# Kernel tuning notes

Measured on AMD Instinct MI355X. Metric: run time of the kernel, lower is better.

Reference implementation:

```python
import jax, jax.numpy as jnp
import numpy as np

TEMPERATURE = 0.5  # init temperature; attn_drop=0.0 so dropout is identity


def setup_inputs() -> dict:
    key = jax.random.key(0)
    k1, k2, k3 = jax.random.split(key, 3)
    B, H, N, D = 4, 8, 2048, 64
    q = jax.random.normal(k1, (B, H, N, D), dtype=jnp.float32)
    k = jax.random.normal(k2, (B, H, N, D), dtype=jnp.float32)
    v = jax.random.normal(k3, (B, H, N, D), dtype=jnp.float32)
    scale = jnp.asarray(D ** -0.5, dtype=jnp.float32)
    return {"q": q, "k": k, "v": v, "scale": scale}


def reference(q, k, v, scale):
    # logits: [B,H,N,N]
    logits = jnp.einsum("bhqd,bhkd->bhqk", q, k) * scale
    # first softmax acts as a soft mask over keys
    soft_mask = jax.nn.softmax(logits / TEMPERATURE, axis=-1)
    # second softmax over masked logits (elementwise product, NOT matmul)
    attn = jax.nn.softmax(logits * soft_mask, axis=-1)
    # dropout with p=0.0 is identity
    out = jnp.einsum("bhqk,bhkd->bhqd", attn, v)
    return out
```

## Files before the change

### kernel.cpp

```cpp
#include <hip/hip_runtime.h>


typedef _Float16 f16;
typedef f16 f16x8 __attribute__((ext_vector_type(8)));
typedef float f32x16 __attribute__((ext_vector_type(16)));

#define MFMA32(a, b, c) __builtin_amdgcn_mfma_f32_32x32x16_f16((a), (b), (c), 0, 0, 0)
#define EXP2(x) __builtin_amdgcn_exp2f(x)

#define N_CTX 2048
#define DH 64
#define KT 64
#define NKT (N_CTX / KT)
#define ROWS 128
#define QS 72
#define HEAD_ELEMS (N_CTX * DH)
#define C2 2.885390081777927f

__device__ inline unsigned pk(float a, float b) {
    typedef __fp16 fp16x2_t __attribute__((ext_vector_type(2)));
    union { fp16x2_t v; unsigned u; } x;
    x.v = __builtin_amdgcn_cvt_pkrtz(a, b);
    return x.u;
}

__device__ inline void load16_lds(const f16* g, f16* l) {
    __builtin_amdgcn_global_load_lds(
        (const __attribute__((address_space(1))) void*)g,
        (__attribute__((address_space(3))) void*)l, 16, 0, 0);
}

__global__ __launch_bounds__(256)
void cvt_kv(const float* __restrict__ k, const float* __restrict__ v,
            f16* __restrict__ ko, f16* __restrict__ vto) {
    __shared__ float Vs[64][65];
    const int bh = blockIdx.x & 31;
    const int kt = blockIdx.x >> 5;
    const int t  = threadIdx.x;
    const float* kb = k + (size_t)bh * HEAD_ELEMS + (size_t)kt * KT * DH;
    f16* kob = ko + (size_t)bh * HEAD_ELEMS + (size_t)kt * KT * DH;
    #pragma unroll
    for (int it = 0; it < 2; ++it) {
        int i = (it * 256 + t) * 8;
        float4 a = *(const float4*)&kb[i];
        float4 b = *(const float4*)&kb[i + 4];
        *(uint4*)&kob[i] = make_uint4(pk(a.x, a.y), pk(a.z, a.w), pk(b.x, b.y), pk(b.z, b.w));
    }
    const float* vb = v + (size_t)bh * HEAD_ELEMS + (size_t)kt * KT * DH;
    #pragma unroll
    for (int it = 0; it < 4; ++it) {
        int idx = it * 256 + t;
        int row = idx >> 4, c4 = idx & 15;
        *(float4*)&Vs[row][c4 * 4] = *(const float4*)&vb[row * DH + c4 * 4];
    }
    __syncthreads();
    int d = t >> 2, sub = t & 3;
    unsigned w[8];
    #pragma unroll
    for (int j = 0; j < 8; ++j) {
        int c = sub * 8 + j;
        w[j] = pk(Vs[c][d], Vs[c + 32][d]);
    }
    f16* ob = vto + (size_t)bh * HEAD_ELEMS + (size_t)d * N_CTX + kt * KT + sub * 16;
    *(uint4*)(ob)     = make_uint4(w[0], w[1], w[2], w[3]);
    *(uint4*)(ob + 8) = make_uint4(w[4], w[5], w[6], w[7]);
}

__global__ __launch_bounds__(256, 2)
void stk_attn_mfma(const float* __restrict__ qg, const f16* __restrict__ kh,
                   const f16* __restrict__ vth, const float* __restrict__ sg,
                   float* __restrict__ og) {
    __shared__ f16 Qs[ROWS * QS];
    __shared__ f16 Ks[2][KT * DH];
    __shared__ f16 Vt[2][DH * KT];
    __shared__ f16 Ps[4][32 * QS];

    const int tid  = threadIdx.x;
    const int wv   = tid >> 6;
    const int lane = tid & 63;
    const int l31  = lane & 31;
    const int lh   = lane >> 5;
    const int bh   = blockIdx.x & 31;
    const int q0   = (blockIdx.x >> 5) * ROWS;
    const float scale2 = sg[0] * C2;

    const float* qb = qg + (size_t)bh * HEAD_ELEMS;
    const f16*   kb = kh + (size_t)bh * HEAD_ELEMS;
    const f16*   vtb = vth + (size_t)bh * HEAD_ELEMS;
    float*       ob = og + (size_t)bh * HEAD_ELEMS;

    #pragma unroll
    for (int it = 0; it < 8; ++it) {
        int idx = it * 256 + tid;
        int row = idx >> 4, c4 = idx & 15;
        float4 v = *(const float4*)&qb[((size_t)(q0 + row)) * DH + c4 * 4];
        *(uint2*)&Qs[row * QS + c4 * 4] =
            make_uint2(pk(v.x * scale2, v.y * scale2), pk(v.z * scale2, v.w * scale2));
    }
    __syncthreads();

    f16x8 aq[4];
    #pragma unroll
    for (int km = 0; km < 4; ++km)
        aq[km] = *(const f16x8*)&Qs[(wv * 32 + l31) * QS + km * 16 + lh * 8];

    const int c0   = (wv * 2) * 64 + lane;
    const int c1   = c0 + 64;
    const int key0 = c0 >> 3, key1 = c1 >> 3;
    const int ks_src0 = key0 * DH + (((c0 & 7) ^ (key0 & 7)) * 8);
    const int ks_src1 = key1 * DH + (((c1 & 7) ^ (key1 & 7)) * 8);
    const long vt_src0 = (long)key0 * N_CTX + (((c0 & 7) ^ (key0 & 7)) * 8);
    const long vt_src1 = (long)key1 * N_CTX + (((c1 & 7) ^ (key1 & 7)) * 8);
    const int dst0 = (wv * 2) * 512, dst1 = dst0 + 512;
    const int x8 = l31 & 7;
    int xo[4];
    #pragma unroll
    for (int km = 0; km < 4; ++km) xo[km] = ((2 * km + lh) ^ x8) * 8;
    const int gb0 = l31 * 64, gb1 = (32 + l31) * 64;
    f16* const ps_wv = &Ps[wv][0];

    float s1[16] = {0};
    load16_lds(kb + ks_src0, &Ks[0][dst0]);
    load16_lds(kb + ks_src1, &Ks[0][dst1]);
    __syncthreads();
    for (int kt = 0; kt < NKT; ++kt) {
        const int cur = kt & 1;
        if (kt + 1 < NKT) {
            const f16* src = kb + (kt + 1) * (KT * DH);
            load16_lds(src + ks_src0, &Ks[cur ^ 1][dst0]);
            load16_lds(src + ks_src1, &Ks[cur ^ 1][dst1]);
        }
        #pragma unroll
        for (int kg = 0; kg < 2; ++kg) {
            const int gb = kg ? gb1 : gb0;
            f32x16 acc;
            #pragma unroll
            for (int i = 0; i < 16; ++i) acc[i] = 0.f;
            #pragma unroll
            for (int km = 0; km < 4; ++km) {
                f16x8 b = *(const f16x8*)&Ks[cur][gb + xo[km]];
                acc = MFMA32(aq[km], b, acc);
            }
            #pragma unroll
            for (int r = 0; r < 16; ++r)
                s1[r] += EXP2(acc[r]);
        }
        __syncthreads();
    }
    float inv1[16];
    #pragma unroll
    for (int r = 0; r < 16; ++r) {
        float v = s1[r];
        v += __shfl_xor(v, 1, 64);
        v += __shfl_xor(v, 2, 64);
        v += __shfl_xor(v, 4, 64);
        v += __shfl_xor(v, 8, 64);
        v += __shfl_xor(v, 16, 64);
        inv1[r] = 0.5f / v;
    }

    float l2[16] = {0};
    f32x16 O0, O1;
    #pragma unroll
    for (int i = 0; i < 16; ++i) { O0[i] = 0.f; O1[i] = 0.f; }

    load16_lds(kb + ks_src0, &Ks[0][dst0]);
    load16_lds(kb + ks_src1, &Ks[0][dst1]);
    load16_lds(vtb + vt_src0, &Vt[0][dst0]);
    load16_lds(vtb + vt_src1, &Vt[0][dst1]);
    __syncthreads();
    for (int kt = 0; kt < NKT; ++kt) {
        const int cur = kt & 1;
        if (kt + 1 < NKT) {
            const f16* src = kb + (kt + 1) * (KT * DH);
            load16_lds(src + ks_src0, &Ks[cur ^ 1][dst0]);
            load16_lds(src + ks_src1, &Ks[cur ^ 1][dst1]);
            load16_lds(vtb + vt_src0 + (kt + 1) * KT, &Vt[cur ^ 1][dst0]);
            load16_lds(vtb + vt_src1 + (kt + 1) * KT, &Vt[cur ^ 1][dst1]);
        }
        f32x16 a0, a1;
        #pragma unroll
        for (int i = 0; i < 16; ++i) { a0[i] = 0.f; a1[i] = 0.f; }
        #pragma unroll
        for (int km = 0; km < 4; ++km) {
            f16x8 b0 = *(const f16x8*)&Ks[cur][gb0 + xo[km]];
            f16x8 b1 = *(const f16x8*)&Ks[cur][gb1 + xo[km]];
            a0 = MFMA32(aq[km], b0, a0);
            a1 = MFMA32(aq[km], b1, a1);
        }
        #pragma unroll
        for (int r = 0; r < 16; ++r) {
            int row_r = (r & 3) + 8 * (r >> 2) + 4 * lh;
            float e10 = EXP2(a0[r]);
            float e20 = EXP2((a0[r] * e10) * inv1[r]);
            float e11 = EXP2(a1[r]);
            float e21 = EXP2((a1[r] * e11) * inv1[r]);
            l2[r] += e20 + e21;
            *(unsigned*)&ps_wv[row_r * QS + 2 * l31] = pk(e20, e21);
        }
        #pragma unroll
        for (int km = 0; km < 4; ++km) {
            f16x8 ap = *(const f16x8*)&ps_wv[l31 * QS + km * 16 + lh * 8];
            f16x8 bv0 = *(const f16x8*)&Vt[cur][gb0 + xo[km]];
            f16x8 bv1 = *(const f16x8*)&Vt[cur][gb1 + xo[km]];
            O0 = MFMA32(ap, bv0, O0);
            O1 = MFMA32(ap, bv1, O1);
        }
        __syncthreads();
    }

    float invl2[16];
    #pragma unroll
    for (int r = 0; r < 16; ++r) {
        float v = l2[r];
        v += __shfl_xor(v, 1, 64);
        v += __shfl_xor(v, 2, 64);
        v += __shfl_xor(v, 4, 64);
        v += __shfl_xor(v, 8, 64);
        v += __shfl_xor(v, 16, 64);
        invl2[r] = 1.0f / v;
    }
    #pragma unroll
    for (int r = 0; r < 16; ++r) {
        int row = q0 + wv * 32 + (r & 3) + 8 * (r >> 2) + 4 * lh;
        ob[(size_t)row * DH + l31]      = O0[r] * invl2[r];
        ob[(size_t)row * DH + 32 + l31] = O1[r] * invl2[r];
    }
}

extern "C" void kernel_launch(void* const* d_in, const int* in_sizes, int n_in,
                              void* d_out, int out_size, void* d_ws, size_t ws_size,
                              hipStream_t stream) {
    const float* q = (const float*)d_in[0];
    const float* k = (const float*)d_in[1];
    const float* v = (const float*)d_in[2];
    const float* s = (const float*)d_in[3];
    float* out = (float*)d_out;
    f16* kf  = (f16*)d_ws;
    f16* vtf = (f16*)((char*)d_ws + 8388608);
    cvt_kv<<<1024, 256, 0, stream>>>(k, v, kf, vtf);
    dim3 grid(32 * 16);
    stk_attn_mfma<<<grid, 256, 0, stream>>>(q, kf, vtf, s, out);
}
```

Measured before the change: 177.5 us.

## Double query rows per block to 256 and alias the P buffer onto Q staging

Each block now processes 256 query rows with 8 waves (512 threads) instead of 128 rows with 4 waves. This halves the grid and halves the K/V tile traffic per query row, since each thread now issues one async LDS load per tile instead of two. The per-wave P buffer is aliased onto the Q staging region, which is no longer needed once Q is held in registers, so LDS use stays within budget. The tradeoff is 256 blocks for a 256-CU-class GPU, which gives only about one block per CU, so latency hiding depends on having 8 waves per block.

```diff
diff --git a/kernel.cpp b/kernel.cpp
--- a/kernel.cpp
+++ b/kernel.cpp
@@ -12,7 +12,7 @@
 #define DH 64
 #define KT 64
 #define NKT (N_CTX / KT)
-#define ROWS 128
+#define ROWS 256
 #define QS 72
 #define HEAD_ELEMS (N_CTX * DH)
 #define C2 2.885390081777927f
@@ -66,14 +66,13 @@
     *(uint4*)(ob + 8) = make_uint4(w[4], w[5], w[6], w[7]);
 }
 
-__global__ __launch_bounds__(256, 2)
+__global__ __launch_bounds__(512, 4)
 void stk_attn_mfma(const float* __restrict__ qg, const f16* __restrict__ kh,
                    const f16* __restrict__ vth, const float* __restrict__ sg,
                    float* __restrict__ og) {
-    __shared__ f16 Qs[ROWS * QS];
+    __shared__ f16 QsPs[ROWS * QS];
     __shared__ f16 Ks[2][KT * DH];
     __shared__ f16 Vt[2][DH * KT];
-    __shared__ f16 Ps[4][32 * QS];
 
     const int tid  = threadIdx.x;
     const int wv   = tid >> 6;
@@ -91,10 +90,10 @@
 
     #pragma unroll
     for (int it = 0; it < 8; ++it) {
-        int idx = it * 256 + tid;
+        int idx = it * 512 + tid;
         int row = idx >> 4, c4 = idx & 15;
         float4 v = *(const float4*)&qb[((size_t)(q0 + row)) * DH + c4 * 4];
-        *(uint2*)&Qs[row * QS + c4 * 4] =
+        *(uint2*)&QsPs[row * QS + c4 * 4] =
             make_uint2(pk(v.x * scale2, v.y * scale2), pk(v.z * scale2, v.w * scale2));
     }
     __syncthreads();
@@ -102,34 +101,28 @@
     f16x8 aq[4];
     #pragma unroll
     for (int km = 0; km < 4; ++km)
-        aq[km] = *(const f16x8*)&Qs[(wv * 32 + l31) * QS + km * 16 + lh * 8];
-
-    const int c0   = (wv * 2) * 64 + lane;
-    const int c1   = c0 + 64;
-    const int key0 = c0 >> 3, key1 = c1 >> 3;
-    const int ks_src0 = key0 * DH + (((c0 & 7) ^ (key0 & 7)) * 8);
-    const int ks_src1 = key1 * DH + (((c1 & 7) ^ (key1 & 7)) * 8);
-    const long vt_src0 = (long)key0 * N_CTX + (((c0 & 7) ^ (key0 & 7)) * 8);
-    const long vt_src1 = (long)key1 * N_CTX + (((c1 & 7) ^ (key1 & 7)) * 8);
-    const int dst0 = (wv * 2) * 512, dst1 = dst0 + 512;
+        aq[km] = *(const f16x8*)&QsPs[(wv * 32 + l31) * QS + km * 16 + lh * 8];
+
+    const int c0   = wv * 64 + lane;
+    const int key0 = c0 >> 3;
+    const int swz  = ((c0 & 7) ^ (key0 & 7)) * 8;
+    const int ks_src0 = key0 * DH + swz;
+    const long vt_src0 = (long)key0 * N_CTX + swz;
+    const int dst0 = wv * 512;
     const int x8 = l31 & 7;
     int xo[4];
     #pragma unroll
     for (int km = 0; km < 4; ++km) xo[km] = ((2 * km + lh) ^ x8) * 8;
     const int gb0 = l31 * 64, gb1 = (32 + l31) * 64;
-    f16* const ps_wv = &Ps[wv][0];
+    f16* const ps_wv = &QsPs[wv * 32 * QS];
 
     float s1[16] = {0};
     load16_lds(kb + ks_src0, &Ks[0][dst0]);
-    load16_lds(kb + ks_src1, &Ks[0][dst1]);
     __syncthreads();
     for (int kt = 0; kt < NKT; ++kt) {
         const int cur = kt & 1;
-        if (kt + 1 < NKT) {
-            const f16* src = kb + (kt + 1) * (KT * DH);
-            load16_lds(src + ks_src0, &Ks[cur ^ 1][dst0]);
-            load16_lds(src + ks_src1, &Ks[cur ^ 1][dst1]);
-        }
+        if (kt + 1 < NKT)
+            load16_lds(kb + (kt + 1) * (KT * DH) + ks_src0, &Ks[cur ^ 1][dst0]);
         #pragma unroll
         for (int kg = 0; kg < 2; ++kg) {
             const int gb = kg ? gb1 : gb0;
@@ -165,18 +158,13 @@
     for (int i = 0; i < 16; ++i) { O0[i] = 0.f; O1[i] = 0.f; }
 
     load16_lds(kb + ks_src0, &Ks[0][dst0]);
-    load16_lds(kb + ks_src1, &Ks[0][dst1]);
     load16_lds(vtb + vt_src0, &Vt[0][dst0]);
-    load16_lds(vtb + vt_src1, &Vt[0][dst1]);
     __syncthreads();
     for (int kt = 0; kt < NKT; ++kt) {
         const int cur = kt & 1;
         if (kt + 1 < NKT) {
-            const f16* src = kb + (kt + 1) * (KT * DH);
-            load16_lds(src + ks_src0, &Ks[cur ^ 1][dst0]);
-            load16_lds(src + ks_src1, &Ks[cur ^ 1][dst1]);
+            load16_lds(kb + (kt + 1) * (KT * DH) + ks_src0, &Ks[cur ^ 1][dst0]);
             load16_lds(vtb + vt_src0 + (kt + 1) * KT, &Vt[cur ^ 1][dst0]);
-            load16_lds(vtb + vt_src1 + (kt + 1) * KT, &Vt[cur ^ 1][dst1]);
         }
         f32x16 a0, a1;
         #pragma unroll
@@ -239,6 +227,6 @@
     f16* kf  = (f16*)d_ws;
     f16* vtf = (f16*)((char*)d_ws + 8388608);
     cvt_kv<<<1024, 256, 0, stream>>>(k, v, kf, vtf);
-    dim3 grid(32 * 16);
-    stk_attn_mfma<<<grid, 256, 0, stream>>>(q, kf, vtf, s, out);
-}
+    dim3 grid(32 * 8);
+    stk_attn_mfma<<<grid, 512, 0, stream>>>(q, kf, vtf, s, out);
+}
```

After: 200.9 us. 13.1% more time.
